# Kernel tuning notes

Measured on AMD Instinct MI355X. Metric: run time of the kernel, lower is better.

The kernel has to match this reference:

```python
import jax, jax.numpy as jnp
import numpy as np

DIM = 64
HEADS = 4
N_NODES = 50000
N_EDGES = 800000
NEG_SLOPE = 0.2


def setup_inputs() -> dict:
    key = jax.random.key(0)
    k1, k2, k3, k4, k5 = jax.random.split(key, 5)
    meta_x = jax.random.normal(k1, (N_NODES, DIM), dtype=jnp.float32)
    meta_edge_index = jax.random.randint(k2, (2, N_EDGES), 0, N_NODES, dtype=jnp.int64)
    # GATConv params: shared source/dest Linear (no bias), per-head attention vecs, output bias.
    glorot = float(np.sqrt(2.0 / (DIM + HEADS * DIM)))
    W = jax.random.normal(k3, (DIM, HEADS * DIM), dtype=jnp.float32) * glorot  # x @ W
    att_src = jax.random.normal(k4, (1, HEADS, DIM), dtype=jnp.float32) * glorot
    att_dst = jax.random.normal(k5, (1, HEADS, DIM), dtype=jnp.float32) * glorot
    bias = jnp.zeros((DIM,), dtype=jnp.float32)
    return {"meta_x": meta_x, "meta_edge_index": meta_edge_index,
            "W": W, "att_src": att_src, "att_dst": att_dst, "bias": bias}


def reference(meta_x, meta_edge_index, W, att_src, att_dst, bias):
    N = meta_x.shape[0]
    # PyG GATConv default: add self-loops
    loops = jnp.arange(N, dtype=meta_edge_index.dtype)
    edge = jnp.concatenate([meta_edge_index, jnp.stack([loops, loops])], axis=1)
    src, dst = edge[0], edge[1]

    x = (meta_x @ W).reshape(N, HEADS, DIM)            # [N, H, C]
    a_src = jnp.sum(x * att_src, axis=-1)              # [N, H]
    a_dst = jnp.sum(x * att_dst, axis=-1)              # [N, H]

    logits = a_src[src] + a_dst[dst]                   # [E, H]
    logits = jax.nn.leaky_relu(logits, NEG_SLOPE)

    # segment softmax over edges grouped by destination node
    seg_max = jax.ops.segment_max(logits, dst, num_segments=N)   # [N, H]
    ex = jnp.exp(logits - seg_max[dst])
    seg_sum = jax.ops.segment_sum(ex, dst, num_segments=N)
    alpha = ex / (seg_sum[dst] + 1e-16)                # [E, H]

    msg = x[src] * alpha[:, :, None]                   # [E, H, C]
    out = jax.ops.segment_sum(msg, dst, num_segments=N)  # [N, H, C]
    # concat=False -> mean over heads, then bias
    return out.mean(axis=1) + bias
```

## Files before the change

### kernel.cpp

```cpp
#include <hip/hip_runtime.h>
#include <hip/hip_bf16.h>
#include <math.h>

#define MAXDEG 64

__device__ __forceinline__ float lrelu(float v) { return v > 0.0f ? v : 0.2f * v; }

__global__ void patt_kernel(const float* __restrict__ W, const float* __restrict__ att_src,
                            const float* __restrict__ att_dst, float* __restrict__ wsrc,
                            float* __restrict__ wdst) {
  int t = threadIdx.x;
  int h = t >> 6, k = t & 63;
  const float* wrow = W + (size_t)k * 256 + h * 64;
  const float* as = att_src + h * 64;
  const float* ad = att_dst + h * 64;
  float ss = 0.f, sd = 0.f;
#pragma unroll
  for (int c = 0; c < 64; ++c) {
    float w = wrow[c];
    ss = fmaf(w, as[c], ss);
    sd = fmaf(w, ad[c], sd);
  }
  wsrc[k * 4 + h] = ss;
  wdst[k * 4 + h] = sd;
}

__global__ void nattn_kernel(const float* __restrict__ x, const float4* __restrict__ wsrc4,
                             const float4* __restrict__ wdst4, float4* __restrict__ asrc4,
                             float4* __restrict__ adst4, __hip_bfloat16* __restrict__ xh,
                             int N) {
  int lane = threadIdx.x & 63;
  int n = blockIdx.x * 4 + (threadIdx.x >> 6);
  if (n >= N) return;
  float xv = x[(size_t)n * 64 + lane];
  xh[(size_t)n * 64 + lane] = __float2bfloat16(xv);
  float4 ws = wsrc4[lane], wd = wdst4[lane];
  float s0 = xv * ws.x, s1 = xv * ws.y, s2 = xv * ws.z, s3 = xv * ws.w;
  float d0 = xv * wd.x, d1 = xv * wd.y, d2 = xv * wd.z, d3 = xv * wd.w;
#pragma unroll
  for (int m = 1; m < 64; m <<= 1) {
    s0 += __shfl_xor(s0, m, 64); s1 += __shfl_xor(s1, m, 64);
    s2 += __shfl_xor(s2, m, 64); s3 += __shfl_xor(s3, m, 64);
    d0 += __shfl_xor(d0, m, 64); d1 += __shfl_xor(d1, m, 64);
    d2 += __shfl_xor(d2, m, 64); d3 += __shfl_xor(d3, m, 64);
  }
  if (lane == 0) {
    asrc4[n] = make_float4(s0, s1, s2, s3);
    adst4[n] = make_float4(d0, d1, d2, d3);
  }
}

__global__ void hist_kernel(const int* __restrict__ ei, int* __restrict__ counts,
                            int E, int N) {
  int e = blockIdx.x * 256 + threadIdx.x;
  int ET = E + N;
  if (e >= ET) return;
  int dst = (e < E) ? ei[(size_t)E + e] : (e - E);
  atomicAdd(&counts[dst], 1);
}

__global__ void scatter_kernel(const int* __restrict__ ei, int* __restrict__ cursor,
                               int* __restrict__ src_sorted, int E, int N) {
  int e = blockIdx.x * 256 + threadIdx.x;
  int ET = E + N;
  if (e >= ET) return;
  int src, dst;
  if (e < E) {
    src = ei[e];
    dst = ei[(size_t)E + e];
  } else {
    src = dst = e - E;
  }
  int pos = atomicAdd(&cursor[dst], 1);
  src_sorted[pos] = src;
}

__global__ void hist4_kernel(const int* __restrict__ ei, int* __restrict__ counts,
                             int E, int N) {
  int i = blockIdx.x * 256 + threadIdx.x;
  int E4 = E >> 2;
  if (i < E4) {
    int4 d = ((const int4*)(ei + E))[i];
    atomicAdd(&counts[d.x], 1);
    atomicAdd(&counts[d.y], 1);
    atomicAdd(&counts[d.z], 1);
    atomicAdd(&counts[d.w], 1);
  } else if (i < E4 + N) {
    atomicAdd(&counts[i - E4], 1);
  }
}

__global__ void scatter8_kernel(const int* __restrict__ ei, int* __restrict__ cursor,
                                int* __restrict__ srt, int E, int N) {
  int slice = blockIdx.x & 7;
  int bid = blockIdx.x >> 3;
  int nb = gridDim.x >> 3;
  int chunk = (N + 7) >> 3;
  int lo = slice * chunk;
  int hi = lo + chunk; if (hi > N) hi = N;
  int E4 = E >> 2;
  const int4* s4p = (const int4*)ei;
  const int4* d4p = (const int4*)(ei + E);
  int stride = nb * 256;
  for (int i = bid * 256 + threadIdx.x; i < E4; i += stride) {
    int4 d4 = d4p[i];
    bool bx = (d4.x >= lo && d4.x < hi), by = (d4.y >= lo && d4.y < hi);
    bool bz = (d4.z >= lo && d4.z < hi), bw = (d4.w >= lo && d4.w < hi);
    if (!(bx || by || bz || bw)) continue;
    int4 s4 = s4p[i];
    if (bx) { int p = atomicAdd(&cursor[d4.x], 1); srt[p] = s4.x; }
    if (by) { int p = atomicAdd(&cursor[d4.y], 1); srt[p] = s4.y; }
    if (bz) { int p = atomicAdd(&cursor[d4.z], 1); srt[p] = s4.z; }
    if (bw) { int p = atomicAdd(&cursor[d4.w], 1); srt[p] = s4.w; }
  }
  for (int n = lo + bid * 256 + threadIdx.x; n < hi; n += stride) {
    int p = atomicAdd(&cursor[n], 1);
    srt[p] = n;
  }
}

__global__ void scanA_kernel(const int* __restrict__ cnt, int* __restrict__ tsum, int N) {
  int b = blockIdx.x, t = threadIdx.x;
  int idx = b * 256 + t;
  int v = (idx < N) ? cnt[idx] : 0;
#pragma unroll
  for (int m = 1; m < 64; m <<= 1) v += __shfl_xor(v, m, 64);
  __shared__ int ws[4];
  if ((t & 63) == 0) ws[t >> 6] = v;
  __syncthreads();
  if (t == 0) tsum[b] = ws[0] + ws[1] + ws[2] + ws[3];
}

__global__ void scanB_kernel(int* __restrict__ tsum, int ntiles) {
  __shared__ int part[256];
  int t = threadIdx.x;
  int carry = 0;
  for (int b0 = 0; b0 < ntiles; b0 += 256) {
    int idx = b0 + t;
    int v = (idx < ntiles) ? tsum[idx] : 0;
    part[t] = v;
    __syncthreads();
    for (int d = 1; d < 256; d <<= 1) {
      int u = (t >= d) ? part[t - d] : 0;
      __syncthreads();
      part[t] += u;
      __syncthreads();
    }
    if (idx < ntiles) tsum[idx] = part[t] - v + carry;
    carry += part[255];
    __syncthreads();
  }
}

__global__ void scanC_kernel(const int* __restrict__ cnt, const int* __restrict__ tsum,
                             int* __restrict__ row, int* __restrict__ cur, int N) {
  __shared__ int part[256];
  int b = blockIdx.x, t = threadIdx.x;
  int idx = b * 256 + t;
  int c = (idx < N) ? cnt[idx] : 0;
  part[t] = c;
  __syncthreads();
  for (int d = 1; d < 256; d <<= 1) {
    int u = (t >= d) ? part[t - d] : 0;
    __syncthreads();
    part[t] += u;
    __syncthreads();
  }
  int exc = part[t] - c + tsum[b];
  if (idx < N) {
    row[idx] = exc;
    cur[idx] = exc;
    if (idx == N - 1) row[N] = exc + c;
  }
}

__global__ __launch_bounds__(256) void agg_kernel(
    const int* __restrict__ srt, const int* __restrict__ row,
    const float4* __restrict__ asrc4, const float4* __restrict__ adst4,
    const __hip_bfloat16* __restrict__ xh, float* __restrict__ agg, int N) {
  __shared__ float4 alL[4][MAXDEG];
  __shared__ int slL[4][MAXDEG];
  int t = threadIdx.x, w = t >> 6, lane = t & 63;
  int n = blockIdx.x * 4 + w;
  if (n >= N) return;
  int start = row[n], end = row[n + 1];
  int deg = end - start;
  float4 ad = adst4[n];
  float t0 = 0.f, t1 = 0.f, t2 = 0.f, t3 = 0.f;
  if (deg <= MAXDEG) {
    for (int b = 0; b < deg; b += 64) {
      if (b + lane < deg) {
        int sl = srt[start + b + lane];
        float4 as = asrc4[sl];
        float4 e;
        e.x = __expf(lrelu(as.x + ad.x));
        e.y = __expf(lrelu(as.y + ad.y));
        e.z = __expf(lrelu(as.z + ad.z));
        e.w = __expf(lrelu(as.w + ad.w));
        alL[w][b + lane] = e;
        slL[w][b + lane] = sl;
        t0 += e.x; t1 += e.y; t2 += e.z; t3 += e.w;
      }
    }
  } else {
    for (int b = start; b < end; b += 64) {
      int idx = b + lane;
      if (idx < end) {
        int sl = srt[idx];
        float4 as = asrc4[sl];
        t0 += __expf(lrelu(as.x + ad.x));
        t1 += __expf(lrelu(as.y + ad.y));
        t2 += __expf(lrelu(as.z + ad.z));
        t3 += __expf(lrelu(as.w + ad.w));
      }
    }
  }
#pragma unroll
  for (int m = 1; m < 64; m <<= 1) {
    t0 += __shfl_xor(t0, m, 64);
    t1 += __shfl_xor(t1, m, 64);
    t2 += __shfl_xor(t2, m, 64);
    t3 += __shfl_xor(t3, m, 64);
  }
  float r0 = 0.25f / (t0 + 1e-16f), r1 = 0.25f / (t1 + 1e-16f);
  float r2 = 0.25f / (t2 + 1e-16f), r3 = 0.25f / (t3 + 1e-16f);
  float a0 = 0.f, a1 = 0.f, a2 = 0.f, a3 = 0.f;
  if (deg <= MAXDEG) {
    int j = 0;
    for (; j + 4 <= deg; j += 4) {
      float4 e0 = alL[w][j], e1 = alL[w][j + 1], e2 = alL[w][j + 2], e3 = alL[w][j + 3];
      int q0 = slL[w][j], q1 = slL[w][j + 1], q2 = slL[w][j + 2], q3 = slL[w][j + 3];
      float v0 = __bfloat162float(xh[(size_t)q0 * 64 + lane]);
      float v1 = __bfloat162float(xh[(size_t)q1 * 64 + lane]);
      float v2 = __bfloat162float(xh[(size_t)q2 * 64 + lane]);
      float v3 = __bfloat162float(xh[(size_t)q3 * 64 + lane]);
      a0 = fmaf(e0.x, v0, a0); a1 = fmaf(e0.y, v0, a1);
      a2 = fmaf(e0.z, v0, a2); a3 = fmaf(e0.w, v0, a3);
      a0 = fmaf(e1.x, v1, a0); a1 = fmaf(e1.y, v1, a1);
      a2 = fmaf(e1.z, v1, a2); a3 = fmaf(e1.w, v1, a3);
      a0 = fmaf(e2.x, v2, a0); a1 = fmaf(e2.y, v2, a1);
      a2 = fmaf(e2.z, v2, a2); a3 = fmaf(e2.w, v2, a3);
      a0 = fmaf(e3.x, v3, a0); a1 = fmaf(e3.y, v3, a1);
      a2 = fmaf(e3.z, v3, a2); a3 = fmaf(e3.w, v3, a3);
    }
    for (; j < deg; ++j) {
      float4 e0 = alL[w][j];
      int q0 = slL[w][j];
      float v0 = __bfloat162float(xh[(size_t)q0 * 64 + lane]);
      a0 = fmaf(e0.x, v0, a0); a1 = fmaf(e0.y, v0, a1);
      a2 = fmaf(e0.z, v0, a2); a3 = fmaf(e0.w, v0, a3);
    }
  } else {
    for (int b = start; b < end; b += 64) {
      int cnt = end - b;
      if (cnt > 64) cnt = 64;
      int idx = b + lane;
      int sl = 0;
      float e0 = 0.f, e1 = 0.f, e2 = 0.f, e3 = 0.f;
      if (idx < end) {
        sl = srt[idx];
        float4 as = asrc4[sl];
        e0 = __expf(lrelu(as.x + ad.x));
        e1 = __expf(lrelu(as.y + ad.y));
        e2 = __expf(lrelu(as.z + ad.z));
        e3 = __expf(lrelu(as.w + ad.w));
      }
      for (int j = 0; j < cnt; ++j) {
        int sj = __shfl(sl, j, 64);
        float b0 = __shfl(e0, j, 64), b1 = __shfl(e1, j, 64);
        float b2 = __shfl(e2, j, 64), b3 = __shfl(e3, j, 64);
        float v = __bfloat162float(xh[(size_t)sj * 64 + lane]);
        a0 = fmaf(b0, v, a0); a1 = fmaf(b1, v, a1);
        a2 = fmaf(b2, v, a2); a3 = fmaf(b3, v, a3);
      }
    }
  }
  float* ao = agg + (size_t)n * 256;
  ao[lane] = a0 * r0;
  ao[64 + lane] = a1 * r1;
  ao[128 + lane] = a2 * r2;
  ao[192 + lane] = a3 * r3;
}

__global__ __launch_bounds__(256) void proj_kernel(
    const float* __restrict__ agg, const float* __restrict__ W,
    const float* __restrict__ bias, float* __restrict__ out, int N) {
  __shared__ float aggL[4][256];
  __shared__ float pL[4][4][64];
  int t = threadIdx.x, w = t >> 6, lane = t & 63;
  float Wreg[64];
#pragma unroll
  for (int k = 0; k < 64; ++k) Wreg[k] = W[(size_t)k * 256 + w * 64 + lane];
  float bv = bias[lane];
  int ngroups = (N + 3) >> 2;
  for (int g = blockIdx.x; g < ngroups; g += gridDim.x) {
    int n0 = g * 4;
    __syncthreads();
    {
      int nn = n0 + w;
      if (nn < N)
        *(float4*)&aggL[w][(t & 63) * 4] =
            *(const float4*)&agg[(size_t)nn * 256 + (t & 63) * 4];
      else
        *(float4*)&aggL[w][(t & 63) * 4] = make_float4(0.f, 0.f, 0.f, 0.f);
    }
    __syncthreads();
    float acc0 = 0.f, acc1 = 0.f, acc2 = 0.f, acc3 = 0.f;
#pragma unroll
    for (int k4 = 0; k4 < 16; ++k4) {
      float4 av0 = *(const float4*)&aggL[0][w * 64 + k4 * 4];
      float4 av1 = *(const float4*)&aggL[1][w * 64 + k4 * 4];
      float4 av2 = *(const float4*)&aggL[2][w * 64 + k4 * 4];
      float4 av3 = *(const float4*)&aggL[3][w * 64 + k4 * 4];
      float w0 = Wreg[k4 * 4 + 0], w1 = Wreg[k4 * 4 + 1];
      float w2 = Wreg[k4 * 4 + 2], w3 = Wreg[k4 * 4 + 3];
      acc0 = fmaf(av0.x, w0, acc0); acc0 = fmaf(av0.y, w1, acc0);
      acc0 = fmaf(av0.z, w2, acc0); acc0 = fmaf(av0.w, w3, acc0);
      acc1 = fmaf(av1.x, w0, acc1); acc1 = fmaf(av1.y, w1, acc1);
      acc1 = fmaf(av1.z, w2, acc1); acc1 = fmaf(av1.w, w3, acc1);
      acc2 = fmaf(av2.x, w0, acc2); acc2 = fmaf(av2.y, w1, acc2);
      acc2 = fmaf(av2.z, w2, acc2); acc2 = fmaf(av2.w, w3, acc2);
      acc3 = fmaf(av3.x, w0, acc3); acc3 = fmaf(av3.y, w1, acc3);
      acc3 = fmaf(av3.z, w2, acc3); acc3 = fmaf(av3.w, w3, acc3);
    }
    pL[w][0][lane] = acc0;
    pL[w][1][lane] = acc1;
    pL[w][2][lane] = acc2;
    pL[w][3][lane] = acc3;
    __syncthreads();
    int nn = n0 + w;
    if (nn < N) {
      out[(size_t)nn * 64 + lane] = pL[0][w][lane] + pL[1][w][lane] +
                                    pL[2][w][lane] + pL[3][w][lane] + bv;
    }
  }
}

__global__ __launch_bounds__(256) void gatout_kernel(
    const int* __restrict__ srt, const int* __restrict__ row,
    const float4* __restrict__ asrc4, const float4* __restrict__ adst4,
    const float* __restrict__ x, const float* __restrict__ W,
    const float* __restrict__ bias, float* __restrict__ out, int N) {
  __shared__ float4 smem4[320];
  float4 (*alL)[MAXDEG] = (float4(*)[MAXDEG])smem4;
  int (*slL)[MAXDEG] = (int(*)[MAXDEG])(smem4 + 256);
  float (*buf)[4][64] = (float(*)[4][64])smem4;
  int t = threadIdx.x, w = t >> 6, lane = t & 63;
  float Wreg[64];
#pragma unroll
  for (int k = 0; k < 64; ++k) Wreg[k] = W[(size_t)k * 256 + w * 64 + lane];
  float bv = bias[lane];
  int ngroups = (N + 3) >> 2;
  for (int g = blockIdx.x; g < ngroups; g += gridDim.x) {
    int n = g * 4 + w;
    float a0 = 0.f, a1 = 0.f, a2 = 0.f, a3 = 0.f;
    float r0 = 0.f, r1 = 0.f, r2 = 0.f, r3 = 0.f;
    __syncthreads();
    if (n < N) {
      int start = row[n], end = row[n + 1];
      int deg = end - start;
      float4 ad = adst4[n];
      float t0 = 0.f, t1 = 0.f, t2 = 0.f, t3 = 0.f;
      if (deg <= MAXDEG) {
        for (int b = 0; b < deg; b += 64) {
          if (b + lane < deg) {
            int sl = srt[start + b + lane];
            float4 as = asrc4[sl];
            float4 e;
            e.x = __expf(lrelu(as.x + ad.x));
            e.y = __expf(lrelu(as.y + ad.y));
            e.z = __expf(lrelu(as.z + ad.z));
            e.w = __expf(lrelu(as.w + ad.w));
            alL[w][b + lane] = e;
            slL[w][b + lane] = sl;
            t0 += e.x; t1 += e.y; t2 += e.z; t3 += e.w;
          }
        }
      } else {
        for (int b = start; b < end; b += 64) {
          int idx = b + lane;
          if (idx < end) {
            int sl = srt[idx];
            float4 as = asrc4[sl];
            t0 += __expf(lrelu(as.x + ad.x));
            t1 += __expf(lrelu(as.y + ad.y));
            t2 += __expf(lrelu(as.z + ad.z));
            t3 += __expf(lrelu(as.w + ad.w));
          }
        }
      }
#pragma unroll
      for (int m = 1; m < 64; m <<= 1) {
        t0 += __shfl_xor(t0, m, 64);
        t1 += __shfl_xor(t1, m, 64);
        t2 += __shfl_xor(t2, m, 64);
        t3 += __shfl_xor(t3, m, 64);
      }
      r0 = 0.25f / (t0 + 1e-16f); r1 = 0.25f / (t1 + 1e-16f);
      r2 = 0.25f / (t2 + 1e-16f); r3 = 0.25f / (t3 + 1e-16f);
      if (deg <= MAXDEG) {
        int j = 0;
        for (; j + 4 <= deg; j += 4) {
          float4 e0 = alL[w][j], e1 = alL[w][j + 1], e2 = alL[w][j + 2], e3 = alL[w][j + 3];
          int q0 = slL[w][j], q1 = slL[w][j + 1], q2 = slL[w][j + 2], q3 = slL[w][j + 3];
          float v0 = x[(size_t)q0 * 64 + lane];
          float v1 = x[(size_t)q1 * 64 + lane];
          float v2 = x[(size_t)q2 * 64 + lane];
          float v3 = x[(size_t)q3 * 64 + lane];
          a0 = fmaf(e0.x, v0, a0); a1 = fmaf(e0.y, v0, a1);
          a2 = fmaf(e0.z, v0, a2); a3 = fmaf(e0.w, v0, a3);
          a0 = fmaf(e1.x, v1, a0); a1 = fmaf(e1.y, v1, a1);
          a2 = fmaf(e1.z, v1, a2); a3 = fmaf(e1.w, v1, a3);
          a0 = fmaf(e2.x, v2, a0); a1 = fmaf(e2.y, v2, a1);
          a2 = fmaf(e2.z, v2, a2); a3 = fmaf(e2.w, v2, a3);
          a0 = fmaf(e3.x, v3, a0); a1 = fmaf(e3.y, v3, a1);
          a2 = fmaf(e3.z, v3, a2); a3 = fmaf(e3.w, v3, a3);
        }
        for (; j < deg; ++j) {
          float4 e0 = alL[w][j];
          int q0 = slL[w][j];
          float v0 = x[(size_t)q0 * 64 + lane];
          a0 = fmaf(e0.x, v0, a0); a1 = fmaf(e0.y, v0, a1);
          a2 = fmaf(e0.z, v0, a2); a3 = fmaf(e0.w, v0, a3);
        }
      } else {
        for (int b = start; b < end; b += 64) {
          int cnt = end - b;
          if (cnt > 64) cnt = 64;
          int idx = b + lane;
          int sl = 0;
          float e0 = 0.f, e1 = 0.f, e2 = 0.f, e3 = 0.f;
          if (idx < end) {
            sl = srt[idx];
            float4 as = asrc4[sl];
            e0 = __expf(lrelu(as.x + ad.x));
            e1 = __expf(lrelu(as.y + ad.y));
            e2 = __expf(lrelu(as.z + ad.z));
            e3 = __expf(lrelu(as.w + ad.w));
          }
          for (int j = 0; j < cnt; ++j) {
            int sj = __shfl(sl, j, 64);
            float b0 = __shfl(e0, j, 64), b1 = __shfl(e1, j, 64);
            float b2 = __shfl(e2, j, 64), b3 = __shfl(e3, j, 64);
            float v = x[(size_t)sj * 64 + lane];
            a0 = fmaf(b0, v, a0); a1 = fmaf(b1, v, a1);
            a2 = fmaf(b2, v, a2); a3 = fmaf(b3, v, a3);
          }
        }
      }
    }
    __syncthreads();
    buf[w][0][lane] = a0 * r0;
    buf[w][1][lane] = a1 * r1;
    buf[w][2][lane] = a2 * r2;
    buf[w][3][lane] = a3 * r3;
    __syncthreads();
    float acc0 = 0.f, acc1 = 0.f, acc2 = 0.f, acc3 = 0.f;
#pragma unroll
    for (int k4 = 0; k4 < 16; ++k4) {
      float4 av0 = *(const float4*)&buf[0][w][k4 * 4];
      float4 av1 = *(const float4*)&buf[1][w][k4 * 4];
      float4 av2 = *(const float4*)&buf[2][w][k4 * 4];
      float4 av3 = *(const float4*)&buf[3][w][k4 * 4];
      float w0 = Wreg[k4 * 4 + 0], w1 = Wreg[k4 * 4 + 1];
      float w2 = Wreg[k4 * 4 + 2], w3 = Wreg[k4 * 4 + 3];
      acc0 = fmaf(av0.x, w0, acc0); acc0 = fmaf(av0.y, w1, acc0);
      acc0 = fmaf(av0.z, w2, acc0); acc0 = fmaf(av0.w, w3, acc0);
      acc1 = fmaf(av1.x, w0, acc1); acc1 = fmaf(av1.y, w1, acc1);
      acc1 = fmaf(av1.z, w2, acc1); acc1 = fmaf(av1.w, w3, acc1);
      acc2 = fmaf(av2.x, w0, acc2); acc2 = fmaf(av2.y, w1, acc2);
      acc2 = fmaf(av2.z, w2, acc2); acc2 = fmaf(av2.w, w3, acc2);
      acc3 = fmaf(av3.x, w0, acc3); acc3 = fmaf(av3.y, w1, acc3);
      acc3 = fmaf(av3.z, w2, acc3); acc3 = fmaf(av3.w, w3, acc3);
    }
    __syncthreads();
    buf[w][0][lane] = acc0;
    buf[w][1][lane] = acc1;
    buf[w][2][lane] = acc2;
    buf[w][3][lane] = acc3;
    __syncthreads();
    if (n < N) {
      out[(size_t)n * 64 + lane] = buf[0][w][lane] + buf[1][w][lane] +
                                   buf[2][w][lane] + buf[3][w][lane] + bv;
    }
  }
}

extern "C" void kernel_launch(void* const* d_in, const int* in_sizes, int n_in,
                              void* d_out, int out_size, void* d_ws, size_t ws_size,
                              hipStream_t stream) {
  const float* meta_x = (const float*)d_in[0];
  const int* ei = (const int*)d_in[1];
  const float* W = (const float*)d_in[2];
  const float* att_src = (const float*)d_in[3];
  const float* att_dst = (const float*)d_in[4];
  const float* bias = (const float*)d_in[5];
  float* out = (float*)d_out;

  int N = in_sizes[0] / 64;
  int E = in_sizes[1] / 2;
  int ET = E + N;

  char* ws = (char*)d_ws;
  size_t off = 0;
  auto alloc = [&](size_t bytes) {
    size_t o = off;
    off += (bytes + 255) & ~(size_t)255;
    return o;
  };
  size_t o_wsrc = alloc(64 * 4 * sizeof(float));
  size_t o_wdst = alloc(64 * 4 * sizeof(float));
  size_t o_asrc = alloc((size_t)N * 4 * sizeof(float));
  size_t o_adst = alloc((size_t)N * 4 * sizeof(float));
  size_t o_cnt = alloc((size_t)N * sizeof(int));
  size_t o_row = alloc(((size_t)N + 1) * sizeof(int));
  size_t o_cur = alloc((size_t)N * sizeof(int));
  size_t o_srt = alloc((size_t)ET * sizeof(int));
  size_t o_ts = alloc((((size_t)N + 255) / 256) * sizeof(int));
  size_t o_xh = alloc((size_t)N * 64 * sizeof(__hip_bfloat16));
  size_t o_agg = alloc((size_t)N * 256 * sizeof(float));
  bool split = (ws_size >= off);

  float* wsrc = (float*)(ws + o_wsrc);
  float* wdst = (float*)(ws + o_wdst);
  float4* asrc4 = (float4*)(ws + o_asrc);
  float4* adst4 = (float4*)(ws + o_adst);
  int* cnt = (int*)(ws + o_cnt);
  int* row = (int*)(ws + o_row);
  int* cur = (int*)(ws + o_cur);
  int* srt = (int*)(ws + o_srt);
  int* tsum = (int*)(ws + o_ts);
  __hip_bfloat16* xh = (__hip_bfloat16*)(ws + o_xh);
  float* aggp = (float*)(ws + o_agg);

  hipMemsetAsync(cnt, 0, (size_t)N * sizeof(int), stream);

  patt_kernel<<<1, 256, 0, stream>>>(W, att_src, att_dst, wsrc, wdst);
  nattn_kernel<<<(N + 3) / 4, 256, 0, stream>>>(meta_x, (const float4*)wsrc,
                                                (const float4*)wdst, asrc4, adst4, xh, N);
  if ((E & 3) == 0) {
    int nt4 = (E >> 2) + N;
    hist4_kernel<<<(nt4 + 255) / 256, 256, 0, stream>>>(ei, cnt, E, N);
  } else {
    hist_kernel<<<(ET + 255) / 256, 256, 0, stream>>>(ei, cnt, E, N);
  }
  int ntiles = (N + 255) / 256;
  scanA_kernel<<<ntiles, 256, 0, stream>>>(cnt, tsum, N);
  scanB_kernel<<<1, 256, 0, stream>>>(tsum, ntiles);
  scanC_kernel<<<ntiles, 256, 0, stream>>>(cnt, tsum, row, cur, N);
  if ((E & 3) == 0) {
    scatter8_kernel<<<2048, 256, 0, stream>>>(ei, cur, srt, E, N);
  } else {
    scatter_kernel<<<(ET + 255) / 256, 256, 0, stream>>>(ei, cur, srt, E, N);
  }
  if (split) {
    agg_kernel<<<(N + 3) / 4, 256, 0, stream>>>(srt, row, asrc4, adst4, xh, aggp, N);
    int ngroups = (N + 3) / 4;
    int pgrid = ngroups < 2048 ? ngroups : 2048;
    proj_kernel<<<pgrid, 256, 0, stream>>>(aggp, W, bias, out, N);
  } else {
    int ngroups = (N + 3) / 4;
    int ggrid = ngroups < 2048 ? ngroups : 2048;
    gatout_kernel<<<ggrid, 256, 0, stream>>>(srt, row, asrc4, adst4, meta_x, W, bias, out, N);
  }
}
```

Baseline: 192.7 us.

## Fuse memset into prep kernel, merge scan passes, store aggregates in bf16

The count-buffer memset is folded into the attention-weight prep kernel, and the separate tile-scan and final-scan kernels become one kernel in which every block redundantly scans the tile sums. This removes launch overhead. The intermediate per-head aggregate buffer is also written and read as bf16 instead of fp32, which halves its traffic between agg_kernel and proj_kernel. The bf16 storage adds rounding error to the aggregated features before projection.

```diff
diff --git a/kernel.cpp b/kernel.cpp
--- a/kernel.cpp
+++ b/kernel.cpp
@@ -6,23 +6,28 @@
 
 __device__ __forceinline__ float lrelu(float v) { return v > 0.0f ? v : 0.2f * v; }
 
-__global__ void patt_kernel(const float* __restrict__ W, const float* __restrict__ att_src,
+__global__ void prep_kernel(int4* __restrict__ cnt4, int n4,
+                            const float* __restrict__ W, const float* __restrict__ att_src,
                             const float* __restrict__ att_dst, float* __restrict__ wsrc,
                             float* __restrict__ wdst) {
-  int t = threadIdx.x;
-  int h = t >> 6, k = t & 63;
-  const float* wrow = W + (size_t)k * 256 + h * 64;
-  const float* as = att_src + h * 64;
-  const float* ad = att_dst + h * 64;
-  float ss = 0.f, sd = 0.f;
-#pragma unroll
-  for (int c = 0; c < 64; ++c) {
-    float w = wrow[c];
-    ss = fmaf(w, as[c], ss);
-    sd = fmaf(w, ad[c], sd);
-  }
-  wsrc[k * 4 + h] = ss;
-  wdst[k * 4 + h] = sd;
+  int idx = blockIdx.x * 256 + threadIdx.x;
+  for (int i = idx; i < n4; i += gridDim.x * 256) cnt4[i] = make_int4(0, 0, 0, 0);
+  if (blockIdx.x == 0) {
+    int t = threadIdx.x;
+    int h = t >> 6, k = t & 63;
+    const float* wrow = W + (size_t)k * 256 + h * 64;
+    const float* as = att_src + h * 64;
+    const float* ad = att_dst + h * 64;
+    float ss = 0.f, sd = 0.f;
+#pragma unroll
+    for (int c = 0; c < 64; ++c) {
+      float w = wrow[c];
+      ss = fmaf(w, as[c], ss);
+      sd = fmaf(w, ad[c], sd);
+    }
+    wsrc[k * 4 + h] = ss;
+    wdst[k * 4 + h] = sd;
+  }
 }
 
 __global__ void nattn_kernel(const float* __restrict__ x, const float4* __restrict__ wsrc4,
@@ -131,6 +136,40 @@
   if (t == 0) tsum[b] = ws[0] + ws[1] + ws[2] + ws[3];
 }
 
+__global__ void scanBC_kernel(const int* __restrict__ cnt, const int* __restrict__ tsum,
+                              int* __restrict__ row, int* __restrict__ cur, int N,
+                              int ntiles) {
+  __shared__ int tl[256];
+  __shared__ int part[256];
+  int b = blockIdx.x, t = threadIdx.x;
+  int tv = (t < ntiles) ? tsum[t] : 0;
+  tl[t] = tv;
+  __syncthreads();
+  for (int d = 1; d < 256; d <<= 1) {
+    int u = (t >= d) ? tl[t - d] : 0;
+    __syncthreads();
+    tl[t] += u;
+    __syncthreads();
+  }
+  int tileoff = (b == 0) ? 0 : tl[b - 1];
+  int idx = b * 256 + t;
+  int c = (idx < N) ? cnt[idx] : 0;
+  part[t] = c;
+  __syncthreads();
+  for (int d = 1; d < 256; d <<= 1) {
+    int u = (t >= d) ? part[t - d] : 0;
+    __syncthreads();
+    part[t] += u;
+    __syncthreads();
+  }
+  int exc = part[t] - c + tileoff;
+  if (idx < N) {
+    row[idx] = exc;
+    cur[idx] = exc;
+    if (idx == N - 1) row[N] = exc + c;
+  }
+}
+
 __global__ void scanB_kernel(int* __restrict__ tsum, int ntiles) {
   __shared__ int part[256];
   int t = threadIdx.x;
@@ -177,7 +216,7 @@
 __global__ __launch_bounds__(256) void agg_kernel(
     const int* __restrict__ srt, const int* __restrict__ row,
     const float4* __restrict__ asrc4, const float4* __restrict__ adst4,
-    const __hip_bfloat16* __restrict__ xh, float* __restrict__ agg, int N) {
+    const __hip_bfloat16* __restrict__ xh, __hip_bfloat16* __restrict__ agg, int N) {
   __shared__ float4 alL[4][MAXDEG];
   __shared__ int slL[4][MAXDEG];
   int t = threadIdx.x, w = t >> 6, lane = t & 63;
@@ -275,15 +314,15 @@
       }
     }
   }
-  float* ao = agg + (size_t)n * 256;
-  ao[lane] = a0 * r0;
-  ao[64 + lane] = a1 * r1;
-  ao[128 + lane] = a2 * r2;
-  ao[192 + lane] = a3 * r3;
+  __hip_bfloat16* ao = agg + (size_t)n * 256;
+  ao[lane] = __float2bfloat16(a0 * r0);
+  ao[64 + lane] = __float2bfloat16(a1 * r1);
+  ao[128 + lane] = __float2bfloat16(a2 * r2);
+  ao[192 + lane] = __float2bfloat16(a3 * r3);
 }
 
 __global__ __launch_bounds__(256) void proj_kernel(
-    const float* __restrict__ agg, const float* __restrict__ W,
+    const __hip_bfloat16* __restrict__ agg, const float* __restrict__ W,
     const float* __restrict__ bias, float* __restrict__ out, int N) {
   __shared__ float aggL[4][256];
   __shared__ float pL[4][4][64];
@@ -298,11 +337,17 @@
     __syncthreads();
     {
       int nn = n0 + w;
-      if (nn < N)
-        *(float4*)&aggL[w][(t & 63) * 4] =
-            *(const float4*)&agg[(size_t)nn * 256 + (t & 63) * 4];
-      else
+      if (nn < N) {
+        ushort4 u = ((const ushort4*)(agg + (size_t)nn * 256))[t & 63];
+        float4 f;
+        f.x = __bfloat162float(*(__hip_bfloat16*)&u.x);
+        f.y = __bfloat162float(*(__hip_bfloat16*)&u.y);
+        f.z = __bfloat162float(*(__hip_bfloat16*)&u.z);
+        f.w = __bfloat162float(*(__hip_bfloat16*)&u.w);
+        *(float4*)&aggL[w][(t & 63) * 4] = f;
+      } else {
         *(float4*)&aggL[w][(t & 63) * 4] = make_float4(0.f, 0.f, 0.f, 0.f);
+      }
     }
     __syncthreads();
     float acc0 = 0.f, acc1 = 0.f, acc2 = 0.f, acc3 = 0.f;
@@ -512,13 +557,13 @@
   size_t o_wdst = alloc(64 * 4 * sizeof(float));
   size_t o_asrc = alloc((size_t)N * 4 * sizeof(float));
   size_t o_adst = alloc((size_t)N * 4 * sizeof(float));
-  size_t o_cnt = alloc((size_t)N * sizeof(int));
+  size_t o_cnt = alloc(((size_t)N + 4) * sizeof(int));
   size_t o_row = alloc(((size_t)N + 1) * sizeof(int));
   size_t o_cur = alloc((size_t)N * sizeof(int));
   size_t o_srt = alloc((size_t)ET * sizeof(int));
   size_t o_ts = alloc((((size_t)N + 255) / 256) * sizeof(int));
   size_t o_xh = alloc((size_t)N * 64 * sizeof(__hip_bfloat16));
-  size_t o_agg = alloc((size_t)N * 256 * sizeof(float));
+  size_t o_agg = alloc((size_t)N * 256 * sizeof(__hip_bfloat16));
   bool split = (ws_size >= off);
 
   float* wsrc = (float*)(ws + o_wsrc);
@@ -531,11 +576,10 @@
   int* srt = (int*)(ws + o_srt);
   int* tsum = (int*)(ws + o_ts);
   __hip_bfloat16* xh = (__hip_bfloat16*)(ws + o_xh);
-  float* aggp = (float*)(ws + o_agg);
-
-  hipMemsetAsync(cnt, 0, (size_t)N * sizeof(int), stream);
-
-  patt_kernel<<<1, 256, 0, stream>>>(W, att_src, att_dst, wsrc, wdst);
+  __hip_bfloat16* aggp = (__hip_bfloat16*)(ws + o_agg);
+
+  int n4 = (N + 4) >> 2;
+  prep_kernel<<<64, 256, 0, stream>>>((int4*)cnt, n4, W, att_src, att_dst, wsrc, wdst);
   nattn_kernel<<<(N + 3) / 4, 256, 0, stream>>>(meta_x, (const float4*)wsrc,
                                                 (const float4*)wdst, asrc4, adst4, xh, N);
   if ((E & 3) == 0) {
@@ -546,8 +590,12 @@
   }
   int ntiles = (N + 255) / 256;
   scanA_kernel<<<ntiles, 256, 0, stream>>>(cnt, tsum, N);
-  scanB_kernel<<<1, 256, 0, stream>>>(tsum, ntiles);
-  scanC_kernel<<<ntiles, 256, 0, stream>>>(cnt, tsum, row, cur, N);
+  if (ntiles <= 256) {
+    scanBC_kernel<<<ntiles, 256, 0, stream>>>(cnt, tsum, row, cur, N, ntiles);
+  } else {
+    scanB_kernel<<<1, 256, 0, stream>>>(tsum, ntiles);
+    scanC_kernel<<<ntiles, 256, 0, stream>>>(cnt, tsum, row, cur, N);
+  }
   if ((E & 3) == 0) {
     scatter8_kernel<<<2048, 256, 0, stream>>>(ei, cur, srt, E, N);
   } else {
```

Result: faster. 186.0 us (-3.5%).
